# Kernel optimization log

Measured on AMD Instinct MI355X. Metric: run time of the kernel, lower is better.

Reference implementation:

```python
import jax, jax.numpy as jnp
from jax import lax
import numpy as np

B, C_IN, H, W = 8, 1024, 64, 64
DI, C_OUT = 512, 1024
BN_EPS = 1e-5


def setup_inputs() -> dict:
    key = jax.random.key(0)
    ks = jax.random.split(key, 5)
    std = 0.01  # torch init.normal_(std=0.01)
    return {
        "x": jax.random.normal(ks[0], (B, C_IN, H, W), jnp.float32),
        "theta_w": jax.random.normal(ks[1], (DI, C_IN), jnp.float32) * std,
        "theta_b": jnp.zeros((DI,), jnp.float32),
        "phi_w": jax.random.normal(ks[2], (DI, C_IN), jnp.float32) * std,
        "phi_b": jnp.zeros((DI,), jnp.float32),
        "g_w": jax.random.normal(ks[3], (DI, C_IN), jnp.float32) * std,
        "g_b": jnp.zeros((DI,), jnp.float32),
        "out_w": jax.random.normal(ks[4], (C_OUT, DI), jnp.float32) * std,
        "out_b": jnp.zeros((C_OUT,), jnp.float32),
        "bn_w": jnp.ones((C_OUT,), jnp.float32),
        "bn_b": jnp.zeros((C_OUT,), jnp.float32),
    }


def _conv1x1(x, w, b):
    # x: [b,c,h,w], w: [o,c] -> [b,o,h,w]
    return jnp.einsum('bchw,oc->bohw', x, w) + b[None, :, None, None]


def reference(x, theta_w, theta_b, phi_w, phi_b, g_w, g_b, out_w, out_b, bn_w, bn_b):
    b, c, h, w = x.shape
    di = theta_w.shape[0]

    theta = _conv1x1(x, theta_w, theta_b).reshape(b, di, h * w)  # [b,di,N]

    # MaxPool2d(kernel=2, stride=2)
    pool = lax.reduce_window(x, -jnp.inf, lax.max,
                             (1, 1, 2, 2), (1, 1, 2, 2), 'VALID')
    phi = _conv1x1(pool, phi_w, phi_b).reshape(b, di, -1)   # [b,di,M]
    g = _conv1x1(pool, g_w, g_b).reshape(b, di, -1)          # [b,di,M]

    # scaled dot-product attention: scores [b,N,M]
    scores = jnp.einsum('bdn,bdm->bnm', theta, phi) * (di ** -0.5)
    p = jax.nn.softmax(scores, axis=-1)

    # t_x = g @ p^T  -> [b,di,N]
    t = jnp.einsum('bdm,bnm->bdn', g, p).reshape(b, di, h, w)

    y = _conv1x1(t, out_w, out_b)  # [b,C_out,h,w]

    # BatchNorm2d (training mode: batch statistics, biased variance)
    mean = jnp.mean(y, axis=(0, 2, 3), keepdims=True)
    var = jnp.var(y, axis=(0, 2, 3), keepdims=True)
    y = (y - mean) * lax.rsqrt(var + BN_EPS)
    y = y * bn_w[None, :, None, None] + bn_b[None, :, None, None]

    return y + x
```

## Files before the change

### kernel.cpp

```cpp
#include <hip/hip_runtime.h>
#include <cstdint>

typedef unsigned short u16;
typedef __attribute__((ext_vector_type(4))) unsigned short u16x4;
typedef __attribute__((ext_vector_type(8))) short short8;
typedef __attribute__((ext_vector_type(4))) float f32x4;

#define DI 512
#define CIN 1024
#define NPIX 4096
#define MPIX 1024

__device__ __forceinline__ float bf2f(u16 u) {
  union { unsigned int i; float f; } v; v.i = ((unsigned int)u) << 16; return v.f;
}
__device__ __forceinline__ u16 f2bf(float f) {
  union { float f; unsigned int i; } v; v.f = f;
  unsigned int r = v.i + 0x7fffu + ((v.i >> 16) & 1u);
  return (u16)(r >> 16);
}
__device__ __forceinline__ void unpack8(uint4 v, float* f) {
  union { unsigned int i; float f; } u;
  u.i = v.x << 16;          f[0] = u.f;
  u.i = v.x & 0xffff0000u;  f[1] = u.f;
  u.i = v.y << 16;          f[2] = u.f;
  u.i = v.y & 0xffff0000u;  f[3] = u.f;
  u.i = v.z << 16;          f[4] = u.f;
  u.i = v.z & 0xffff0000u;  f[5] = u.f;
  u.i = v.w << 16;          f[6] = u.f;
  u.i = v.w & 0xffff0000u;  f[7] = u.f;
}

__device__ __forceinline__ void gload16(const u16* g, u16* l) {
  __builtin_amdgcn_global_load_lds(
      (const __attribute__((address_space(1))) void*)g,
      (__attribute__((address_space(3))) void*)l, 16, 0, 0);
}

__global__ __launch_bounds__(256) void cvt4_kernel(
    const float* __restrict__ s0, const float* __restrict__ s1,
    const float* __restrict__ s2, const float* __restrict__ s3,
    u16* __restrict__ d0, u16* __restrict__ d1,
    u16* __restrict__ d2, u16* __restrict__ d3) {
  int i = blockIdx.x * 256 + threadIdx.x;
  int sel = i >> 17;
  int j = i & 131071;
  const float* src = sel == 0 ? s0 : sel == 1 ? s1 : sel == 2 ? s2 : s3;
  u16* dst = sel == 0 ? d0 : sel == 1 ? d1 : sel == 2 ? d2 : d3;
  float4 v = *(const float4*)(src + (long)j * 4);
  u16x4 w;
  w[0] = f2bf(v.x); w[1] = f2bf(v.y); w[2] = f2bf(v.z); w[3] = f2bf(v.w);
  *(u16x4*)(dst + (long)j * 4) = w;
}

__global__ __launch_bounds__(256) void transpose_pool_kernel(
    const float* __restrict__ x, u16* __restrict__ xT, u16* __restrict__ poolT) {
  __shared__ u16 tile[64][136];
  const int b = blockIdx.z;
  const int n0 = blockIdx.x * 128, c0 = blockIdx.y * 64;
  const float* xb = x + (long)b * CIN * NPIX;
  u16* xTb = xT + (long)b * NPIX * CIN;
  const int t = threadIdx.x;
  const int tc = t >> 5, tn = (t & 31) * 4;
  #pragma unroll
  for (int i = 0; i < 8; i++) {
    int c = tc + i * 8;
    float4 v = *(const float4*)(xb + (long)(c0 + c) * NPIX + n0 + tn);
    u16x4 w;
    w[0] = f2bf(v.x); w[1] = f2bf(v.y); w[2] = f2bf(v.z); w[3] = f2bf(v.w);
    *(u16x4*)&tile[c][tn] = w;
  }
  __syncthreads();
  const int tn2 = t >> 4, tc2 = (t & 15) * 4;
  #pragma unroll
  for (int i = 0; i < 8; i++) {
    int n = tn2 + i * 16;
    u16x4 w;
    w[0] = tile[tc2 + 0][n];
    w[1] = tile[tc2 + 1][n];
    w[2] = tile[tc2 + 2][n];
    w[3] = tile[tc2 + 3][n];
    *(u16x4*)(xTb + (long)(n0 + n) * CIN + c0 + tc2) = w;
  }
  const int j = t & 31, g = t >> 5;
  u16 r[8] __attribute__((aligned(16)));
  #pragma unroll
  for (int k = 0; k < 8; k++) {
    const int c = g * 8 + k;
    const unsigned d0 = *(const unsigned*)&tile[c][2 * j];
    const unsigned d1 = *(const unsigned*)&tile[c][64 + 2 * j];
    float m0 = fmaxf(bf2f((u16)(d0 & 0xffffu)), bf2f((u16)(d0 >> 16)));
    float m1 = fmaxf(bf2f((u16)(d1 & 0xffffu)), bf2f((u16)(d1 >> 16)));
    r[k] = f2bf(fmaxf(m0, m1));
  }
  *(uint4*)(poolT + ((long)b * MPIX + blockIdx.x * 32 + j) * CIN + c0 + g * 8) =
      *(uint4*)r;
}

template<int OM, bool HAS_BIAS, bool HAS_SHIFT, bool HAS_EXP, bool HAS_PSUM2,
         bool HAS_CSP>
__global__ __launch_bounds__(512, 2)
void gemm256(const u16* __restrict__ A, const u16* __restrict__ B,
             void* __restrict__ Cv,
             const float* __restrict__ bias, long sBias,
             const float* __restrict__ cs, long sCS,
             const float* __restrict__ shift, long sShift,
             float* __restrict__ psum_out,
             float scale, int M, int N, int K, long sA, long sB, long sC)
{
  A += blockIdx.z * sA;
  B += blockIdx.z * sB;
  if (HAS_BIAS) bias += blockIdx.z * sBias;
  if (HAS_CSP) cs += blockIdx.z * sCS;
  if (HAS_SHIFT) shift += blockIdx.z * sShift;
  const int bm = blockIdx.y * 256, bn = blockIdx.x * 256;
  __shared__ __align__(16) u16 smem[65536];
  __shared__ float psum[4][256];
  __shared__ float psumq[4][256];
  __shared__ float invs[256];
  const int tid = threadIdx.x;
  const int lane = tid & 63, wave = tid >> 6;
  const int wr = wave >> 2, wc = wave & 3;
  const int lr = lane & 15, q = lane >> 4, sx = lane & 7;
  f32x4 acc[8][4] = {};

  if (HAS_CSP && tid < 256) {
    float ssum = 0.f;
    #pragma unroll
    for (int xx = 0; xx < 4; xx++) ssum += cs[xx * 4096 + bn + tid];
    invs[tid] = 1.0f / ssum;
  }

  const int swz = ((lane & 7) ^ (lane >> 3)) * 8;
  const long grow = 32 * wave + (lane >> 3);
  const u16* Ag = A + ((long)bm + grow) * K + swz;
  const u16* Bg = B + ((long)bn + grow) * K + swz;
  const int niter = K >> 6;

  #pragma unroll
  for (int i = 0; i < 4; i++) {
    gload16(Ag + (long)(8 * i) * K, &smem[(32 * wave + 8 * i) * 64]);
    gload16(Bg + (long)(8 * i) * K, &smem[16384 + (32 * wave + 8 * i) * 64]);
  }

  for (int t = 0; t < niter; ++t) {
    const int s = t & 1;
    __builtin_amdgcn_s_barrier();
    __builtin_amdgcn_sched_barrier(0);
    if (t + 1 < niter) {
      const long kofs = (long)(t + 1) * 64;
      const int db = (s ^ 1) * 32768;
      #pragma unroll
      for (int i = 0; i < 4; i++) {
        gload16(Ag + (long)(8 * i) * K + kofs, &smem[db + (32 * wave + 8 * i) * 64]);
        gload16(Bg + (long)(8 * i) * K + kofs,
                &smem[db + 16384 + (32 * wave + 8 * i) * 64]);
      }
      asm volatile("s_waitcnt vmcnt(8)" ::: "memory");
    } else {
      asm volatile("s_waitcnt vmcnt(0)" ::: "memory");
    }
    __builtin_amdgcn_s_barrier();
    __builtin_amdgcn_sched_barrier(0);
    const int bA = s * 32768, bB = s * 32768 + 16384;
    #pragma unroll
    for (int kk = 0; kk < 2; kk++) {
      short8 bv[4];
      #pragma unroll
      for (int ci = 0; ci < 4; ci++)
        bv[ci] = *(const short8*)&smem[bB + (wc * 64 + ci * 16 + lr) * 64 +
                                       (((kk << 2) + q) ^ sx) * 8];
      #pragma unroll
      for (int ri = 0; ri < 8; ri++) {
        short8 av = *(const short8*)&smem[bA + (wr * 128 + ri * 16 + lr) * 64 +
                                          (((kk << 2) + q) ^ sx) * 8];
        #pragma unroll
        for (int ci = 0; ci < 4; ci++)
          acc[ri][ci] = __builtin_amdgcn_mfma_f32_16x16x32_bf16(
              av, bv[ci], acc[ri][ci], 0, 0, 0);
      }
    }
  }
  __syncthreads();

  const int dr = (lane >> 4) * 4;
  float invc[4];
  if (HAS_CSP) {
    #pragma unroll
    for (int ci = 0; ci < 4; ci++) invc[ci] = invs[wc * 64 + ci * 16 + lr];
  }
  float rowsum[8][4], rowsq[8][4];
  if (HAS_EXP || HAS_PSUM2) {
    #pragma unroll
    for (int ri = 0; ri < 8; ri++)
      #pragma unroll
      for (int r = 0; r < 4; r++) { rowsum[ri][r] = 0.f; rowsq[ri][r] = 0.f; }
  }
  #pragma unroll
  for (int ri = 0; ri < 8; ri++) {
    const int rowl = wr * 128 + ri * 16 + dr;
    const int rowb = bm + rowl;
    float bvs[4] = {0.f, 0.f, 0.f, 0.f};
    float shv[4] = {0.f, 0.f, 0.f, 0.f};
    if (HAS_BIAS) {
      #pragma unroll
      for (int r = 0; r < 4; r++) bvs[r] = bias[rowb + r];
    }
    if (HAS_SHIFT) {
      #pragma unroll
      for (int r = 0; r < 4; r++) shv[r] = shift[rowb + r];
    }
    #pragma unroll
    for (int ci = 0; ci < 4; ci++) {
      const int coll = wc * 64 + ci * 16 + lr;
      float v[4];
      #pragma unroll
      for (int r = 0; r < 4; r++) {
        float tv = acc[ri][ci][r] * scale;
        if (HAS_CSP) tv *= invc[ci];
        if (HAS_SHIFT) tv -= shv[r];
        if (HAS_BIAS) tv += bvs[r];
        if (HAS_EXP) tv = expf(tv);
        if (HAS_EXP || HAS_PSUM2) rowsum[ri][r] += tv;
        if (HAS_PSUM2) rowsq[ri][r] += tv * tv;
        v[r] = tv;
      }
      if (OM == 1) {
        u16x4 w;
        #pragma unroll
        for (int r = 0; r < 4; r++) w[r] = f2bf(v[r]);
        unsigned bo = (unsigned)((coll * 256 + rowl) * 2) ^ ((coll & 7) << 4);
        *(u16x4*)((char*)smem + bo) = w;
      } else {
        #pragma unroll
        for (int r = 0; r < 4; r++) smem[(rowl + r) * 256 + coll] = f2bf(v[r]);
      }
    }
  }
  if (HAS_EXP || HAS_PSUM2) {
    #pragma unroll
    for (int msk = 1; msk < 16; msk <<= 1)
      #pragma unroll
      for (int ri = 0; ri < 8; ri++)
        #pragma unroll
        for (int r = 0; r < 4; r++) {
          rowsum[ri][r] += __shfl_xor(rowsum[ri][r], msk);
          if (HAS_PSUM2) rowsq[ri][r] += __shfl_xor(rowsq[ri][r], msk);
        }
    if ((lane & 15) == 0) {
      #pragma unroll
      for (int ri = 0; ri < 8; ri++)
        #pragma unroll
        for (int r = 0; r < 4; r++) {
          psum[wc][wr * 128 + ri * 16 + dr + r] = rowsum[ri][r];
          if (HAS_PSUM2) psumq[wc][wr * 128 + ri * 16 + dr + r] = rowsq[ri][r];
        }
    }
  }
  __syncthreads();
  u16* C = (u16*)Cv + blockIdx.z * sC;
  if (OM == 1) {
    #pragma unroll
    for (int i = 0; i < 16; i++) {
      const int chunk = i * 512 + tid;
      const int coll = chunk >> 5, rq = chunk & 31;
      unsigned bo = (unsigned)(coll * 512 + rq * 16) ^ ((coll & 7) << 4);
      uint4 w = *(const uint4*)((const char*)smem + bo);
      *(uint4*)(C + (long)(bn + coll) * M + bm + rq * 8) = w;
    }
  } else {
    #pragma unroll
    for (int i = 0; i < 16; i++) {
      const int chunk = i * 512 + tid;
      const int row = chunk >> 5, cq = chunk & 31;
      uint4 w = *(const uint4*)(smem + row * 256 + cq * 8);
      *(uint4*)(C + (long)(bm + row) * N + bn + cq * 8) = w;
    }
  }
  if ((HAS_EXP || HAS_PSUM2) && tid < 256) {
    if (HAS_EXP)
      psum_out[((long)blockIdx.z * gridDim.x + blockIdx.x) * 4096 + bm + tid] =
          psum[0][tid] + psum[1][tid] + psum[2][tid] + psum[3][tid];
    if (HAS_PSUM2) {
      const long blk = ((long)blockIdx.z * gridDim.y + blockIdx.y) * gridDim.x
                       + blockIdx.x;
      psum_out[blk * 512 + tid] =
          psum[0][tid] + psum[1][tid] + psum[2][tid] + psum[3][tid];
      psum_out[blk * 512 + 256 + tid] =
          psumq[0][tid] + psumq[1][tid] + psumq[2][tid] + psumq[3][tid];
    }
  }
}

template<int OM, bool HAS_BIAS, bool HAS_CS, bool HAS_SHIFT, bool HAS_EXP,
         bool HAS_PSUM2, bool HAS_CSP>
__global__ __launch_bounds__(256)
void gemm_tn(const u16* __restrict__ A, const u16* __restrict__ B,
             void* __restrict__ Cv, void* __restrict__ Cv2,
             const float* __restrict__ bias, const float* __restrict__ bias2,
             long sBias,
             const float* __restrict__ cs, long sCS,
             const float* __restrict__ shift, long sShift,
             float* __restrict__ psum_out,
             float scale, int M, int N, int K, long sA, long sB, long sC)
{
  A += blockIdx.z * sA;
  B += blockIdx.z * sB;
  if (HAS_BIAS) bias += blockIdx.z * sBias;
  if (HAS_CS || HAS_CSP) cs += blockIdx.z * sCS;
  if (HAS_SHIFT) shift += blockIdx.z * sShift;
  const int bm = blockIdx.y * 128;
  const int bn = blockIdx.x * 128;
  __shared__ __align__(16) u16 smem[128 * 128];
  u16* As = smem;
  u16* Bs = smem + 128 * 64;
  __shared__ float psum[4][128];
  const int tid = threadIdx.x;
  const int lane = tid & 63;
  const int wave = tid >> 6;
  const int wm = (wave >> 1) * 64;
  const int wn = (wave & 1) * 64;
  const int lr = lane & 15;
  const int q  = lane >> 4;
  const int sxor = lane & 7;
  const bool gps = (OM == 3) && (bm >= 512);
  f32x4 acc[4][4] = {};

  if (HAS_CSP) {
    if (tid < 128) {
      float s = 0.f;
      #pragma unroll
      for (int xx = 0; xx < 8; xx++) s += cs[xx * 4096 + bn + tid];
      psum[0][tid] = 1.0f / s;
    }
  }

  const int swz = ((lane & 7) ^ (lane >> 3)) * 8;
  const long grow = 32 * wave + (lane >> 3);
  const u16* Ag = A + ((long)bm + grow) * K + swz;
  const u16* Bg = B + ((long)bn + grow) * K + swz;

  for (int kt = 0; kt < K; kt += 64) {
    __syncthreads();
    #pragma unroll
    for (int i = 0; i < 4; i++) {
      gload16(Ag + (long)(8 * i) * K + kt, &As[(wave * 4 + i) * 512]);
      gload16(Bg + (long)(8 * i) * K + kt, &Bs[(wave * 4 + i) * 512]);
    }
    __syncthreads();
    #pragma unroll
    for (int kk = 0; kk < 2; kk++) {
      short8 av[4], bv[4];
      #pragma unroll
      for (int mi = 0; mi < 4; mi++)
        av[mi] = *(const short8*)&As[(wm + mi * 16 + lr) * 64 +
                                     (((kk << 2) + q) ^ sxor) * 8];
      #pragma unroll
      for (int ni = 0; ni < 4; ni++)
        bv[ni] = *(const short8*)&Bs[(wn + ni * 16 + lr) * 64 +
                                     (((kk << 2) + q) ^ sxor) * 8];
      #pragma unroll
      for (int mi = 0; mi < 4; mi++) {
        #pragma unroll
        for (int ni = 0; ni < 4; ni++)
          acc[mi][ni] = __builtin_amdgcn_mfma_f32_16x16x32_bf16(
              av[mi], bv[ni], acc[mi][ni], 0, 0, 0);
      }
    }
  }

  float invc[4];
  if (HAS_CSP) {
    #pragma unroll
    for (int ni = 0; ni < 4; ni++) invc[ni] = psum[0][wn + ni * 16 + lr];
  }
  __syncthreads();
  const int dr = (lane >> 4) * 4;
  const bool trans_out = (OM == 1) || (OM == 3 && !gps);
  float rowsum[4][4];
  float rowsq[4][4];
  if (HAS_EXP || HAS_PSUM2 || gps) {
    #pragma unroll
    for (int mi = 0; mi < 4; mi++)
      #pragma unroll
      for (int r = 0; r < 4; r++) { rowsum[mi][r] = 0.f; rowsq[mi][r] = 0.f; }
  }
  const float* bp = (OM == 3 && gps) ? bias2 - 512 : bias;
  #pragma unroll
  for (int mi = 0; mi < 4; mi++) {
    const int rowl = wm + mi * 16 + dr;
    const int rowb = bm + rowl;
    float bvs[4] = {0.f, 0.f, 0.f, 0.f};
    float shv[4] = {0.f, 0.f, 0.f, 0.f};
    if (HAS_BIAS) {
      #pragma unroll
      for (int r = 0; r < 4; r++) bvs[r] = bp[rowb + r];
    }
    if (HAS_SHIFT) {
      #pragma unroll
      for (int r = 0; r < 4; r++) shv[r] = shift[rowb + r];
    }
    #pragma unroll
    for (int ni = 0; ni < 4; ni++) {
      const int coll = wn + ni * 16 + lr;
      const float csv = HAS_CSP ? invc[ni] : (HAS_CS ? cs[bn + coll] : 1.0f);
      float v[4];
      #pragma unroll
      for (int r = 0; r < 4; r++) {
        float t = acc[mi][ni][r] * scale;
        if (HAS_CS || HAS_CSP) t *= csv;
        if (HAS_SHIFT) t -= shv[r];
        if (HAS_BIAS) t += bvs[r];
        if (HAS_EXP) t = expf(t);
        if (HAS_EXP || HAS_PSUM2 || gps) rowsum[mi][r] += t;
        if (HAS_PSUM2) rowsq[mi][r] += t * t;
        v[r] = t;
      }
      if (trans_out) {
        u16x4 w;
        #pragma unroll
        for (int r = 0; r < 4; r++) w[r] = f2bf(v[r]);
        unsigned bo = (unsigned)((coll * 128 + rowl) * 2) ^ ((coll & 7) << 4);
        *(u16x4*)((char*)smem + bo) = w;
      } else {
        #pragma unroll
        for (int r = 0; r < 4; r++) smem[(rowl + r) * 128 + coll] = f2bf(v[r]);
      }
    }
  }
  if (HAS_EXP || HAS_PSUM2 || gps) {
    #pragma unroll
    for (int msk = 1; msk < 16; msk <<= 1)
      #pragma unroll
      for (int mi = 0; mi < 4; mi++)
        #pragma unroll
        for (int r = 0; r < 4; r++) {
          rowsum[mi][r] += __shfl_xor(rowsum[mi][r], msk);
          if (HAS_PSUM2) rowsq[mi][r] += __shfl_xor(rowsq[mi][r], msk);
        }
    if ((lane & 15) == 0) {
      #pragma unroll
      for (int mi = 0; mi < 4; mi++)
        #pragma unroll
        for (int r = 0; r < 4; r++) {
          psum[wave & 1][wm + mi * 16 + dr + r] = rowsum[mi][r];
          if (HAS_PSUM2) psum[2 + (wave & 1)][wm + mi * 16 + dr + r] = rowsq[mi][r];
        }
    }
  }
  __syncthreads();
  if (trans_out) {
    const int Ms = (OM == 3) ? 512 : M;
    u16* C = (u16*)Cv + blockIdx.z * sC;
    #pragma unroll
    for (int i = 0; i < 8; i++) {
      const int chunk = i * 256 + tid;
      const int coll = chunk >> 4, rq = chunk & 15;
      unsigned bo = (unsigned)(coll * 256 + rq * 16) ^ ((coll & 7) << 4);
      uint4 w = *(const uint4*)((const char*)smem + bo);
      *(uint4*)(C + (long)(bn + coll) * Ms + bm + rq * 8) = w;
    }
  } else {
    u16* C = (OM == 3) ? (u16*)Cv2 + blockIdx.z * sC : (u16*)Cv + blockIdx.z * sC;
    const int rbase = (OM == 3) ? bm - 512 : bm;
    #pragma unroll
    for (int i = 0; i < 8; i++) {
      const int chunk = i * 256 + tid;
      const int row = chunk >> 4, cq = chunk & 15;
      uint4 w = *(const uint4*)(smem + row * 128 + cq * 8);
      *(uint4*)(C + (long)(rbase + row) * N + bn + cq * 8) = w;
    }
  }
  if (HAS_EXP || HAS_PSUM2 || gps) {
    if (tid < 128) {
      if (HAS_EXP)
        psum_out[((long)blockIdx.z * gridDim.x + blockIdx.x) * 4096 + bm + tid] =
            psum[0][tid] + psum[1][tid];
      if (HAS_PSUM2) {
        const long blk = ((long)blockIdx.z * gridDim.y + blockIdx.y) * gridDim.x
                         + blockIdx.x;
        psum_out[blk * 256 + tid] = psum[0][tid] + psum[1][tid];
        psum_out[blk * 256 + 128 + tid] = psum[2][tid] + psum[3][tid];
      }
      if (gps)
        psum_out[((long)blockIdx.z * gridDim.x + blockIdx.x) * 512 +
                 (bm - 512) + tid] = psum[0][tid] + psum[1][tid];
    }
  }
}

__global__ __launch_bounds__(256) void gbar_kernel(const float* __restrict__ g_ps,
                                                   float* __restrict__ gbar) {
  const int idx = blockIdx.x * 256 + threadIdx.x;
  const int b = idx >> 9, d = idx & 511;
  const float* p = g_ps + (long)b * 8 * 512 + d;
  float s = 0.f;
  #pragma unroll
  for (int xx = 0; xx < 8; xx++) s += p[(long)xx * 512];
  gbar[idx] = s * (1.0f / 1024.0f);
}

__global__ __launch_bounds__(256) void c0_kernel(const float* __restrict__ out_w,
                                                 const float* __restrict__ out_b,
                                                 const float* __restrict__ gbar,
                                                 float* __restrict__ c0) {
  const int idx = blockIdx.x * 4 + (threadIdx.x >> 6);
  const int lane = threadIdx.x & 63;
  const int b = idx >> 10, c = idx & 1023;
  const int d0 = lane * 8;
  float4 w0 = *(const float4*)(out_w + (long)c * DI + d0);
  float4 w1 = *(const float4*)(out_w + (long)c * DI + d0 + 4);
  float4 g0 = *(const float4*)(gbar + (long)b * DI + d0);
  float4 g1 = *(const float4*)(gbar + (long)b * DI + d0 + 4);
  float s = w0.x * g0.x + w0.y * g0.y + w0.z * g0.z + w0.w * g0.w
          + w1.x * g1.x + w1.y * g1.y + w1.z * g1.z + w1.w * g1.w;
  #pragma unroll
  for (int off = 32; off > 0; off >>= 1) s += __shfl_xor(s, off);
  if (lane == 0) c0[idx] = out_b[c] + s;
}

__global__ __launch_bounds__(256) void stats2_kernel(const float* __restrict__ partial,
                                                     const float* __restrict__ c0,
                                                     float* __restrict__ stats) {
  const int co = blockIdx.x * 256 + threadIdx.x;
  const int by = co >> 8, r = co & 255;
  float sd = 0.f, sd2 = 0.f, sbc = 0.f;
  for (int b = 0; b < 8; b++) {
    float sb = 0.f, qb = 0.f;
    #pragma unroll
    for (int bx = 0; bx < 16; bx++) {
      const long blk = (((long)b * 4 + by) * 16 + bx) * 512;
      sb += partial[blk + r];
      qb += partial[blk + 256 + r];
    }
    sd += sb; sd2 += qb;
    sbc += c0[b * 1024 + co] * sb;
  }
  float sc0 = 0.f, sc02 = 0.f;
  #pragma unroll
  for (int b = 0; b < 8; b++) {
    float c = c0[b * 1024 + co];
    sc0 += c; sc02 += c * c;
  }
  stats[co] = 4096.0f * sc0 + sd;
  stats[1024 + co] = 4096.0f * sc02 + 2.0f * sbc + sd2;
}

__global__ __launch_bounds__(256) void final_kernel(const u16* __restrict__ dy,
    const float* __restrict__ x, const float* __restrict__ stats,
    const float* __restrict__ c0,
    const float* __restrict__ bnw, const float* __restrict__ bnb,
    float* __restrict__ out) {
  const int bc = blockIdx.x;
  const int co = bc & 1023;
  const float mean = stats[co] * (1.0f / 32768.0f);
  const float var = stats[1024 + co] * (1.0f / 32768.0f) - mean * mean;
  const float inv = rsqrtf(var + 1e-5f) * bnw[co];
  const float addc = bnb[co] - mean * inv + c0[bc] * inv;
  const long base = (long)bc * 4096;
  const int t = threadIdx.x;
  #pragma unroll
  for (int i = 0; i < 2; i++) {
    const long off = base + (long)(i * 256 + t) * 8;
    uint4 v = *(const uint4*)(dy + off);
    float f[8]; unpack8(v, f);
    const float4 x0 = *(const float4*)(x + off);
    const float4 x1 = *(const float4*)(x + off + 4);
    float4 o0, o1;
    o0.x = f[0] * inv + addc + x0.x;
    o0.y = f[1] * inv + addc + x0.y;
    o0.z = f[2] * inv + addc + x0.z;
    o0.w = f[3] * inv + addc + x0.w;
    o1.x = f[4] * inv + addc + x1.x;
    o1.y = f[5] * inv + addc + x1.y;
    o1.z = f[6] * inv + addc + x1.z;
    o1.w = f[7] * inv + addc + x1.w;
    *(float4*)(out + off) = o0;
    *(float4*)(out + off + 4) = o1;
  }
}

extern "C" void kernel_launch(void* const* d_in, const int* in_sizes, int n_in,
                              void* d_out, int out_size, void* d_ws, size_t ws_size,
                              hipStream_t stream) {
  (void)in_sizes; (void)n_in; (void)out_size; (void)ws_size;
  const float* x       = (const float*)d_in[0];
  const float* theta_w = (const float*)d_in[1];
  const float* theta_b = (const float*)d_in[2];
  const float* phi_w   = (const float*)d_in[3];
  const float* phi_b   = (const float*)d_in[4];
  const float* g_w     = (const float*)d_in[5];
  const float* g_b     = (const float*)d_in[6];
  const float* out_w   = (const float*)d_in[7];
  const float* out_b   = (const float*)d_in[8];
  const float* bn_w    = (const float*)d_in[9];
  const float* bn_b    = (const float*)d_in[10];
  float* out = (float*)d_out;
  char* ws = (char*)d_ws;
  const size_t MB = 1024 * 1024;

  u16* xT     = (u16*)(ws + 0 * MB);
  u16* poolT  = (u16*)(ws + 64 * MB);
  u16* w_th   = (u16*)(ws + 80 * MB);
  u16* w_ph   = (u16*)(ws + 81 * MB);
  u16* w_g    = (u16*)(ws + 82 * MB);
  u16* thetaT = (u16*)(ws + 84 * MB);
  u16* phiT   = (u16*)(ws + 116 * MB);
  u16* g_n    = (u16*)(ws + 124 * MB);
  u16* e      = (u16*)(ws + 132 * MB);
  u16* tT     = (u16*)(ws + 196 * MB);
  u16* w_out  = (u16*)(ws + 228 * MB);
  float* gbar  = (float*)(ws + 229 * MB);
  float* c0b   = (float*)(ws + 229 * MB + 16384);
  float* stats = (float*)(ws + 229 * MB + 49152);
  float* partial = (float*)(ws + 230 * MB);
  float* partial2 = (float*)(ws + 231 * MB);
  float* g_ps = (float*)(ws + 233 * MB);
  u16* dy = xT;

  cvt4_kernel<<<2048, 256, 0, stream>>>(theta_w, phi_w, g_w, out_w,
                                        w_th, w_ph, w_g, w_out);
  transpose_pool_kernel<<<dim3(32, 16, 8), 256, 0, stream>>>(x, xT, poolT);
  gemm256<1, true, false, false, false, false>
      <<<dim3(16, 2, 8), 512, 0, stream>>>(
      w_th, xT, thetaT, theta_b, 0L, nullptr, 0L, nullptr, 0L, nullptr,
      1.0f, 512, 4096, 1024, 0L, (long)NPIX * CIN, (long)NPIX * DI);
  gemm_tn<3, true, false, false, false, false, false>
      <<<dim3(8, 8, 8), 256, 0, stream>>>(
      w_ph, poolT, phiT, g_n, phi_b, g_b, 0L, nullptr, 0L, nullptr, 0L,
      g_ps, 1.0f, 1024, 1024, 1024, 0L, (long)MPIX * CIN, (long)MPIX * DI);
  gbar_kernel<<<16, 256, 0, stream>>>(g_ps, gbar);
  c0_kernel<<<2048, 256, 0, stream>>>(out_w, out_b, gbar, c0b);
  gemm256<0, false, false, true, false, false>
      <<<dim3(4, 16, 8), 512, 0, stream>>>(
      thetaT, phiT, e, nullptr, 0L, nullptr, 0L, nullptr, 0L, partial,
      0.044194173824159216f, 4096, 1024, 512,
      (long)NPIX * DI, (long)MPIX * DI, (long)NPIX * MPIX);
  gemm256<1, false, true, false, false, true>
      <<<dim3(16, 2, 8), 512, 0, stream>>>(
      g_n, e, tT, nullptr, 0L, partial, 16384L, gbar, 512L, nullptr,
      1.0f, 512, 4096, 1024,
      (long)DI * MPIX, (long)NPIX * MPIX, (long)NPIX * DI);
  gemm256<0, false, false, false, true, false>
      <<<dim3(16, 4, 8), 512, 0, stream>>>(
      w_out, tT, dy, nullptr, 0L, nullptr, 0L, nullptr, 0L, partial2,
      1.0f, 1024, 4096, 512, 0L, (long)NPIX * DI, (long)1024 * NPIX);
  stats2_kernel<<<4, 256, 0, stream>>>(partial2, c0b, stats);
  final_kernel<<<8192, 256, 0, stream>>>(dy, x, stats, c0b, bn_w, bn_b, out);
}
```

Measured before the change: 343.8 us.

## Restructure GEMM mainloop into fine-grained eight-phase pipeline with split-K LDS layout

Replaces the double-buffered 64-wide K loop with an unrolled loop over 128-wide K steps, split into eight phases. Each phase issues one small global-to-LDS load stage, waits on a tuned vmcnt, and runs a quarter of the MFMA work between barriers. It changes the LDS layout to 32-element K halves with a new XOR swizzle and raises wave priority around MFMA blocks. The aim is to interleave loads with compute more finely and hide memory latency. The cost is many more barriers per K step and the assumption that K is a multiple of 128.

```diff
diff --git a/kernel.cpp b/kernel.cpp
--- a/kernel.cpp
+++ b/kernel.cpp
@@ -35,6 +35,21 @@
   __builtin_amdgcn_global_load_lds(
       (const __attribute__((address_space(1))) void*)g,
       (__attribute__((address_space(3))) void*)l, 16, 0, 0);
+}
+
+template<int N> __device__ __forceinline__ void wait_vmcnt() {
+  asm volatile("s_waitcnt vmcnt(%0)" :: "n"(N) : "memory");
+}
+__device__ __forceinline__ void phase_begin() {
+  __builtin_amdgcn_s_barrier();
+  __builtin_amdgcn_sched_barrier(0);
+  asm volatile("" ::: "memory");
+}
+__device__ __forceinline__ void phase_end() {
+  asm volatile("s_waitcnt lgkmcnt(0)" ::: "memory");
+  __builtin_amdgcn_sched_barrier(0);
+  __builtin_amdgcn_s_barrier();
+  __builtin_amdgcn_sched_barrier(0);
 }
 
 __global__ __launch_bounds__(256) void cvt4_kernel(
@@ -121,66 +136,88 @@
   const int tid = threadIdx.x;
   const int lane = tid & 63, wave = tid >> 6;
   const int wr = wave >> 2, wc = wave & 3;
-  const int lr = lane & 15, q = lane >> 4, sx = lane & 7;
+  const int lr = lane & 15, q = lane >> 4;
   f32x4 acc[8][4] = {};
 
-  if (HAS_CSP && tid < 256) {
-    float ssum = 0.f;
-    #pragma unroll
-    for (int xx = 0; xx < 4; xx++) ssum += cs[xx * 4096 + bn + tid];
-    invs[tid] = 1.0f / ssum;
-  }
-
-  const int swz = ((lane & 7) ^ (lane >> 3)) * 8;
-  const long grow = 32 * wave + (lane >> 3);
-  const u16* Ag = A + ((long)bm + grow) * K + swz;
-  const u16* Bg = B + ((long)bn + grow) * K + swz;
-  const int niter = K >> 6;
-
-  #pragma unroll
-  for (int i = 0; i < 4; i++) {
-    gload16(Ag + (long)(8 * i) * K, &smem[(32 * wave + 8 * i) * 64]);
-    gload16(Bg + (long)(8 * i) * K, &smem[16384 + (32 * wave + 8 * i) * 64]);
-  }
-
-  for (int t = 0; t < niter; ++t) {
-    const int s = t & 1;
-    __builtin_amdgcn_s_barrier();
+  if (HAS_CSP) {
+    if (tid < 256) {
+      float ssum = 0.f;
+      #pragma unroll
+      for (int xx = 0; xx < 4; xx++) ssum += cs[xx * 4096 + bn + tid];
+      invs[tid] = 1.0f / ssum;
+    }
+    wait_vmcnt<0>();
     __builtin_amdgcn_sched_barrier(0);
-    if (t + 1 < niter) {
-      const long kofs = (long)(t + 1) * 64;
-      const int db = (s ^ 1) * 32768;
-      #pragma unroll
-      for (int i = 0; i < 4; i++) {
-        gload16(Ag + (long)(8 * i) * K + kofs, &smem[db + (32 * wave + 8 * i) * 64]);
-        gload16(Bg + (long)(8 * i) * K + kofs,
-                &smem[db + 16384 + (32 * wave + 8 * i) * 64]);
-      }
-      asm volatile("s_waitcnt vmcnt(8)" ::: "memory");
-    } else {
-      asm volatile("s_waitcnt vmcnt(0)" ::: "memory");
-    }
-    __builtin_amdgcn_s_barrier();
-    __builtin_amdgcn_sched_barrier(0);
-    const int bA = s * 32768, bB = s * 32768 + 16384;
-    #pragma unroll
-    for (int kk = 0; kk < 2; kk++) {
-      short8 bv[4];
-      #pragma unroll
-      for (int ci = 0; ci < 4; ci++)
-        bv[ci] = *(const short8*)&smem[bB + (wc * 64 + ci * 16 + lr) * 64 +
-                                       (((kk << 2) + q) ^ sx) * 8];
-      #pragma unroll
-      for (int ri = 0; ri < 8; ri++) {
-        short8 av = *(const short8*)&smem[bA + (wr * 128 + ri * 16 + lr) * 64 +
-                                          (((kk << 2) + q) ^ sx) * 8];
-        #pragma unroll
-        for (int ci = 0; ci < 4; ci++)
-          acc[ri][ci] = __builtin_amdgcn_mfma_f32_16x16x32_bf16(
-              av, bv[ci], acc[ri][ci], 0, 0, 0);
-      }
-    }
-  }
+  }
+
+  const int srow = 32 * wave + (lane >> 2);
+  const int sk = (((lane & 3) ^ ((lane >> 3) & 3))) * 8;
+  const u16* Abase = A + ((long)bm + srow) * K + sk;
+  const u16* Bbase = B + ((long)bn + srow) * K + sk;
+  const int rswz = (q ^ ((lr >> 1) & 3)) * 8;
+  const int aoff = (wr * 128 + lr) * 32 + rswz;
+  const int boff = 16384 + (wc * 64 + lr) * 32 + rswz;
+
+#define SA(T_, KK_) { const u16* g_ = Abase + (long)(T_) * 64 + (KK_) * 32; \
+    u16* d_ = &smem[(((T_) & 1)) * 32768 + (KK_) * 8192 + wave * 1024]; \
+    gload16(g_, d_); gload16(g_ + 16 * (long)K, d_ + 512); }
+#define SB(T_, KK_) { const u16* g_ = Bbase + (long)(T_) * 64 + (KK_) * 32; \
+    u16* d_ = &smem[(((T_) & 1)) * 32768 + 16384 + (KK_) * 8192 + wave * 1024]; \
+    gload16(g_, d_); gload16(g_ + 16 * (long)K, d_ + 512); }
+#define CQ(SLOT, KK, RI0, LOADBV) { \
+    const int qb_ = (SLOT) * 32768 + (KK) * 8192; \
+    if (LOADBV) { \
+      _Pragma("unroll") \
+      for (int ci_ = 0; ci_ < 4; ci_++) \
+        bv[ci_] = *(const short8*)&smem[qb_ + boff + ci_ * 512]; \
+    } \
+    short8 av_[4]; \
+    _Pragma("unroll") \
+    for (int r_ = 0; r_ < 4; r_++) \
+      av_[r_] = *(const short8*)&smem[qb_ + aoff + ((RI0) + r_) * 512]; \
+    __builtin_amdgcn_s_setprio(1); \
+    _Pragma("unroll") \
+    for (int r_ = 0; r_ < 4; r_++) \
+      _Pragma("unroll") \
+      for (int ci_ = 0; ci_ < 4; ci_++) \
+        acc[(RI0) + r_][ci_] = __builtin_amdgcn_mfma_f32_16x16x32_bf16( \
+            av_[r_], bv[ci_], acc[(RI0) + r_][ci_], 0, 0, 0); \
+    __builtin_amdgcn_s_setprio(0); }
+#define PH(VM, STG, SLOT, KK, RI0, LOADBV) \
+    STG; wait_vmcnt<VM>(); phase_begin(); CQ(SLOT, KK, RI0, LOADBV); phase_end();
+
+  const int niter2 = K >> 7;
+  short8 bv[4];
+
+  SA(0, 0); SB(0, 0); SA(0, 1); SB(0, 1); SA(1, 0); SB(1, 0);
+
+  for (int u = 0; u < niter2 - 1; ++u) {
+    const int t1 = 2 * u + 1, t2 = 2 * u + 2, t3 = 2 * u + 3;
+    PH(10, SA(t1, 1), 0, 0, 0, 1)
+    PH(10, SB(t1, 1), 0, 0, 4, 0)
+    PH(10, SA(t2, 0), 0, 1, 0, 1)
+    PH(10, SB(t2, 0), 0, 1, 4, 0)
+    PH(10, SA(t2, 1), 1, 0, 0, 1)
+    PH(10, SB(t2, 1), 1, 0, 4, 0)
+    PH(10, SA(t3, 0), 1, 1, 0, 1)
+    PH(10, SB(t3, 0), 1, 1, 4, 0)
+  }
+  {
+    const int t1 = 2 * (niter2 - 1) + 1;
+    PH(10, SA(t1, 1), 0, 0, 0, 1)
+    PH(10, SB(t1, 1), 0, 0, 4, 0)
+    PH(8,  ((void)0), 0, 1, 0, 1)
+    PH(6,  ((void)0), 0, 1, 4, 0)
+    PH(4,  ((void)0), 1, 0, 0, 1)
+    PH(2,  ((void)0), 1, 0, 4, 0)
+    PH(0,  ((void)0), 1, 1, 0, 1)
+    PH(0,  ((void)0), 1, 1, 4, 0)
+  }
+#undef SA
+#undef SB
+#undef CQ
+#undef PH
+
   __syncthreads();
 
   const int dr = (lane >> 4) * 4;
```

New measurement: 344.7 us. No clear change (+0.3%).
